# Kernel tuning notes

Hardware: AMD Instinct MI355X
Metric: run time of the kernel (lower is better)

The kernel has to match this reference:

```python
import jax, jax.numpy as jnp
import numpy as np
from jax import lax

BZ, CAPACITY, SEQ_LEN, IN_VAR, N_EDGES = 64, 134, 288, 16, 96


def setup_inputs() -> dict:
    key = jax.random.key(0)
    ks = jax.random.split(key, 9)
    s_gcn = 1.0 / np.sqrt(SEQ_LEN)
    s_conv = 1.0 / np.sqrt(IN_VAR * 3)
    s_fc = 1.0 / np.sqrt(2 * IN_VAR)
    return {
        "src": jax.random.normal(ks[0], (BZ, CAPACITY, SEQ_LEN, IN_VAR), dtype=jnp.float32),
        "feature_edge_index": jax.random.randint(ks[1], (2, N_EDGES), 0, IN_VAR, dtype=jnp.int32),
        # SAGEConv(seq_len, seq_len): out = lin_l(mean_neighbors) + lin_r(x); lin_l has bias
        "Wl": jax.random.uniform(ks[2], (SEQ_LEN, SEQ_LEN), jnp.float32, -s_gcn, s_gcn),
        "Wr": jax.random.uniform(ks[3], (SEQ_LEN, SEQ_LEN), jnp.float32, -s_gcn, s_gcn),
        "b_gcn": jax.random.uniform(ks[4], (SEQ_LEN,), jnp.float32, -s_gcn, s_gcn),
        "conv1_w": jax.random.uniform(ks[5], (IN_VAR, IN_VAR, 3), jnp.float32, -s_conv, s_conv),
        "conv2_w": jax.random.uniform(ks[6], (IN_VAR, IN_VAR, 5), jnp.float32, -s_conv, s_conv),
        "fc_w": jax.random.uniform(ks[7], (IN_VAR, 2 * IN_VAR), jnp.float32, -s_fc, s_fc),
        "fc_b": jax.random.uniform(ks[8], (IN_VAR,), jnp.float32, -s_fc, s_fc),
    }


def reference(src, feature_edge_index, Wl, Wr, b_gcn, conv1_w, conv2_w, fc_w, fc_b):
    bz, cap, S, F = src.shape  # [bz, capacity, seq_len, in_var]
    B = bz * cap
    # node features for the feature graph: [B, in_var, seq_len]
    x2 = src.transpose(0, 1, 3, 2).reshape(B, F, S)
    e_src, e_dst = feature_edge_index[0], feature_edge_index[1]
    # SAGEConv mean aggregation over shared edge_index, vectorized across B graphs
    gathered = x2[:, e_src, :]                                   # [B, E, S]
    agg = jnp.zeros_like(x2).at[:, e_dst, :].add(gathered)       # [B, F, S]
    deg = jnp.zeros((F,), x2.dtype).at[e_dst].add(1.0)
    mean = agg / jnp.maximum(deg, 1.0)[None, :, None]
    feat = (jnp.einsum('bns,ts->bnt', mean, Wl)
            + jnp.einsum('bns,ts->bnt', x2, Wr) + b_gcn)          # [B, F, S]
    fea_fea = feat.reshape(bz, cap, F, S).transpose(0, 1, 3, 2)   # [bz,cap,S,F]
    # dual temporal Conv1d branches (same padding, no bias) on [B, F, S]
    dn = ('NCH', 'OIH', 'NCH')
    c1 = lax.conv_general_dilated(x2, conv1_w, (1,), [(1, 1)], dimension_numbers=dn)
    c2 = lax.conv_general_dilated(x2, conv2_w, (2,), [(2, 2)][:1] * 1, dimension_numbers=dn) if False else lax.conv_general_dilated(x2, conv2_w, (1,), [(2, 2)], dimension_numbers=dn)
    temporal = (c1 + c2).transpose(0, 2, 1).reshape(bz, cap, S, F)
    com = jnp.concatenate([fea_fea, temporal], axis=-1)           # [bz,cap,S,2F]
    com = jnp.einsum('bcsf,of->bcso', com, fc_w) + fc_b
    # dropout is identity in eval mode
    return src + com
```

## Files before the change

kernel.cpp:

```cpp
#include <hip/hip_runtime.h>
#include <hip/hip_bf16.h>

typedef short short8 __attribute__((ext_vector_type(8)));
typedef float float4v __attribute__((ext_vector_type(4)));
typedef unsigned short ushort4v __attribute__((ext_vector_type(4)));

#define BTOT 8576
#define SEQ 288
#define NF 16
#define NB 3
#define SPN 296
#define XTROWS 294
#define XT_USH (XTROWS * 16)
#define XN_USH (16 * SPN)
#define PBN (XT_USH + XN_USH)
#define WCVW 104

__device__ __forceinline__ unsigned short f2b(float f) {
    union { float f; unsigned u; } v; v.f = f;
    unsigned r = v.u + 0x7FFF + ((v.u >> 16) & 1);
    return (unsigned short)(r >> 16);
}
__device__ __forceinline__ float b2f(unsigned short u) {
    union { unsigned u; float f; } v; v.u = ((unsigned)u) << 16; return v.f;
}

__global__ void wcast_kernel(const float* __restrict__ a, const float* __restrict__ b,
                             unsigned short* __restrict__ o) {
    int i = blockIdx.x * 256 + threadIdx.x;
    o[i]         = f2b(a[i]);
    o[82944 + i] = f2b(b[i]);
}

template<int WPRE>
__device__ __forceinline__ short8 ldw(const unsigned short* __restrict__ wb,
                                      const float* __restrict__ wf, int idx) {
    if (WPRE) {
        return *(const short8*)&wb[idx];
    } else {
        const float* p = &wf[idx];
        float4 w0 = *(const float4*)p, w1 = *(const float4*)(p + 4);
        short8 a;
        a[0] = (short)f2b(w0.x); a[1] = (short)f2b(w0.y);
        a[2] = (short)f2b(w0.z); a[3] = (short)f2b(w0.w);
        a[4] = (short)f2b(w1.x); a[5] = (short)f2b(w1.y);
        a[6] = (short)f2b(w1.z); a[7] = (short)f2b(w1.w);
        return a;
    }
}

#define LDB(KK9, B_) do {                                                      \
    const int s0_ = (KK9) * 32;                                                \
    (B_)[0] = *(const short8*)&xsN0[li * SPN + s0_ + 8 * g];                   \
    (B_)[1] = *(const short8*)&xsN1[li * SPN + s0_ + 8 * g];                   \
    (B_)[2] = *(const short8*)&xsN2[li * SPN + s0_ + 8 * g];                   \
} while (0)

#define LDA(WT_, WF_, KK9, A_) do {                                            \
    const int s0_ = (KK9) * 32;                                                \
    _Pragma("unroll")                                                          \
    for (int m_ = 0; m_ < 3; ++m_)                                             \
        if (m_ < nt) (A_)[m_] = ldw<WPRE>(WT_, WF_, arow[m_] + s0_ + 8 * g);   \
} while (0)

#define MFK(A_, B_) do {                                                       \
    _Pragma("unroll")                                                          \
    for (int m_ = 0; m_ < 3; ++m_)                                             \
        if (m_ < nt) {                                                         \
            acc[m_][0] = __builtin_amdgcn_mfma_f32_16x16x32_bf16((A_)[m_], (B_)[0], acc[m_][0], 0, 0, 0); \
            acc[m_][1] = __builtin_amdgcn_mfma_f32_16x16x32_bf16((A_)[m_], (B_)[1], acc[m_][1], 0, 0, 0); \
            acc[m_][2] = __builtin_amdgcn_mfma_f32_16x16x32_bf16((A_)[m_], (B_)[2], acc[m_][2], 0, 0, 0); \
        }                                                                      \
} while (0)

#define GEMM9(WT_, WF_) do {                                                   \
    short8 aC[3], aN[3];                                                       \
    LDA(WT_, WF_, 0, aC);                                                      \
    LDA(WT_, WF_, 1, aN);                                                      \
    _Pragma("unroll")                                                          \
    for (int kk = 0; kk < 9; ++kk) {                                           \
        short8 bb[NB];                                                         \
        LDB(kk, bb);                                                           \
        if (kk & 1) { MFK(aN, bb); if (kk < 7) LDA(WT_, WF_, kk + 2, aN); }    \
        else        { MFK(aC, bb); if (kk < 7) LDA(WT_, WF_, kk + 2, aC); }    \
    }                                                                          \
} while (0)

template<int WPRE>
__global__ __launch_bounds__(512, 4) void stconv_mfma(
    const float* __restrict__ src,
    const int*   __restrict__ eidx,
    const float* __restrict__ Wlf,
    const float* __restrict__ Wrf,
    const unsigned short* __restrict__ Wbf,
    const float* __restrict__ bgcn,
    const float* __restrict__ cw1g,
    const float* __restrict__ cw2g,
    const float* __restrict__ fcwg,
    const float* __restrict__ fcbg,
    float*       __restrict__ out)
{
    __shared__ unsigned short pool[NB * PBN];
    __shared__ unsigned short wcv[16 * WCVW];
    __shared__ unsigned short fcwB[16 * 40];
    __shared__ unsigned short MB[16 * 40];
    __shared__ float bg[SEQ];
    __shared__ float Msc[256];
    __shared__ float fcb[16];

    const int tid  = threadIdx.x;
    const int wav  = tid >> 6;
    const int lane = tid & 63;
    const int li   = lane & 15;
    const int g    = lane >> 4;
    const int b0   = blockIdx.x * NB;

    int bid[NB];
    #pragma unroll
    for (int n = 0; n < NB; ++n) bid[n] = (b0 + n < BTOT) ? (b0 + n) : (BTOT - 1);

    if (tid < 256) Msc[tid] = 0.0f;
    for (int i = tid; i < 16 * 40; i += 512) MB[i] = 0;
    for (int i = tid; i < 16 * WCVW; i += 512) wcv[i] = 0;
    if (tid < 288) {
        int nb2 = tid / 96, r2 = tid % 96;
        int r = r2 >> 4, f = r2 & 15;
        int row = (r < 2) ? r : 288 + r;
        pool[nb2 * PBN + row * 16 + f] = 0;
    }
    __syncthreads();

    if (tid < 96) atomicAdd(&Msc[eidx[96 + tid] * 16 + eidx[tid]], 1.0f);
    {
        #pragma unroll
        for (int i = 0; i < 2; ++i) {
            int u = i * 512 + tid;
            if (u < NB * 288) {
                int nbu = u / 288, blk = u % 288;
                const float* srcb = src + (size_t)bid[0] * 0  + (size_t)((nbu == 0) ? bid[0] : (nbu == 1) ? bid[1] : bid[2]) * (SEQ * NF);
                unsigned short* xsTu = pool + nbu * PBN;
                unsigned short* xsNu = pool + nbu * PBN + XT_USH;
                int s0 = (blk >> 2) * 4, f0 = (blk & 3) * 4;
                ushort4v h[4];
                #pragma unroll
                for (int r = 0; r < 4; ++r) {
                    float4 v = *(const float4*)(srcb + (s0 + r) * 16 + f0);
                    h[r][0] = f2b(v.x); h[r][1] = f2b(v.y);
                    h[r][2] = f2b(v.z); h[r][3] = f2b(v.w);
                    *(ushort4v*)&xsTu[(s0 + r + 2) * 16 + f0] = h[r];
                }
                #pragma unroll
                for (int c = 0; c < 4; ++c) {
                    ushort4v w;
                    w[0] = h[0][c]; w[1] = h[1][c]; w[2] = h[2][c]; w[3] = h[3][c];
                    *(ushort4v*)&xsNu[(f0 + c) * SPN + s0] = w;
                }
            }
        }
    }
    for (int j = tid; j < 1280; j += 512) {
        int fo = j / 80, rem = j % 80, fi = rem / 5, d = rem % 5;
        float t = cw2g[(fo * 16 + fi) * 5 + d];
        if (d >= 1 && d <= 3) t += cw1g[(fo * 16 + fi) * 3 + (d - 1)];
        wcv[fo * WCVW + d * 16 + fi] = f2b(t);
    }
    if (tid < 512) fcwB[(tid >> 5) * 40 + (tid & 31)] = f2b(fcwg[tid]);
    if (tid < SEQ) bg[tid] = bgcn[tid];
    if (tid < 16) fcb[tid] = fcbg[tid];
    __syncthreads();

    if (tid < 16) {
        float deg = 0.0f;
        #pragma unroll
        for (int f = 0; f < 16; ++f) deg += Msc[tid * 16 + f];
        float inv = 1.0f / fmaxf(deg, 1.0f);
        #pragma unroll
        for (int f = 0; f < 16; ++f) MB[tid * 40 + f] = f2b(Msc[tid * 16 + f] * inv);
    }
    __syncthreads();

    const int t2 = (wav == 0) ? 16 : ((wav == 5) ? 17 : -1);
    const int nt = (t2 >= 0) ? 3 : 2;
    const int tts[3] = {wav, wav + 8, t2};
    const int arow[3] = {(tts[0] * 16 + li) * 288, (tts[1] * 16 + li) * 288,
                         (t2 >= 0) ? ((t2 * 16 + li) * 288) : 0};

    const unsigned short* WblT = Wbf;
    const unsigned short* WbrT = Wbf + 288 * 288;
    const unsigned short* xsN0 = pool + 0 * PBN + XT_USH;
    const unsigned short* xsN1 = pool + 1 * PBN + XT_USH;
    const unsigned short* xsN2 = pool + 2 * PBN + XT_USH;

    float4v acc[3][NB];

    #pragma unroll
    for (int m = 0; m < 3; ++m)
        if (m < nt) {
            #pragma unroll
            for (int r = 0; r < 4; ++r) {
                float bv = bg[tts[m] * 16 + 4 * g + r];
                #pragma unroll
                for (int n = 0; n < NB; ++n) acc[m][n][r] = bv;
            }
        }
    GEMM9(WbrT, Wrf);
    __syncthreads();

    {
        short8 bm = *(const short8*)&MB[li * 40 + 8 * g];
        #pragma unroll
        for (int it = 0; it < 7; ++it) {
            int u = wav + 8 * it;
            if (u < NB * 18) {
                int nbu = u / 18, st = u % 18;
                unsigned short* xsTu = pool + nbu * PBN;
                unsigned short* msNu = pool + nbu * PBN + XT_USH;
                int s0 = st * 16;
                short8 a = {0, 0, 0, 0, 0, 0, 0, 0};
                if (g < 2) a = *(const short8*)&xsTu[(s0 + li + 2) * 16 + 8 * g];
                float4v c = {0.f, 0.f, 0.f, 0.f};
                c = __builtin_amdgcn_mfma_f32_16x16x32_bf16(a, bm, c, 0, 0, 0);
                ushort4v p;
                #pragma unroll
                for (int r = 0; r < 4; ++r) p[r] = f2b(c[r]);
                *(ushort4v*)&msNu[li * SPN + s0 + 4 * g] = p;
            }
        }
    }
    __syncthreads();

    GEMM9(WblT, Wlf);

    ushort4v p5o[3][NB];
    #pragma unroll
    for (int m = 0; m < 3; ++m)
        if (m < nt) {
            #pragma unroll
            for (int n = 0; n < NB; ++n) {
                #pragma unroll
                for (int r = 0; r < 4; ++r)
                    p5o[m][n][r] = f2b(acc[m][n][r]);
            }
        }

    ushort4v p6o[7];
    {
        short8 cb0 = *(const short8*)&wcv[li * WCVW + 0  + 8 * g];
        short8 cb1 = *(const short8*)&wcv[li * WCVW + 32 + 8 * g];
        short8 cb2 = *(const short8*)&wcv[li * WCVW + 64 + 8 * g];
        const int fi0   = (g & 1) * 8;
        const int dbase = g >> 1;
        #pragma unroll
        for (int it = 0; it < 7; ++it) {
            int u = wav + 8 * it;
            if (u < NB * 18) {
                int nbu = u / 18, st = u % 18;
                const unsigned short* xsTu = pool + nbu * PBN;
                int s0 = st * 16;
                int rbase = (s0 + li + dbase) * 16 + fi0;
                short8 a0 = *(const short8*)&xsTu[rbase];
                short8 a1 = *(const short8*)&xsTu[rbase + 32];
                short8 a2 = *(const short8*)&xsTu[rbase + 64];
                float4v c = {0.f, 0.f, 0.f, 0.f};
                c = __builtin_amdgcn_mfma_f32_16x16x32_bf16(a0, cb0, c, 0, 0, 0);
                c = __builtin_amdgcn_mfma_f32_16x16x32_bf16(a1, cb1, c, 0, 0, 0);
                c = __builtin_amdgcn_mfma_f32_16x16x32_bf16(a2, cb2, c, 0, 0, 0);
                #pragma unroll
                for (int r = 0; r < 4; ++r) p6o[it][r] = f2b(c[r]);
            }
        }
    }

    ushort4v res16[7];
    #pragma unroll
    for (int it = 0; it < 7; ++it) {
        int u = wav + 8 * it;
        if (u < NB * 18) {
            int nbu = u / 18, st = u % 18;
            const unsigned short* xsTu = pool + nbu * PBN;
            int s0 = st * 16;
            #pragma unroll
            for (int r = 0; r < 4; ++r)
                res16[it][r] = xsTu[(s0 + 4 * g + r + 2) * 16 + li];
        }
    }
    __syncthreads();

    {
        #pragma unroll
        for (int m = 0; m < 3; ++m)
            if (m < nt) {
                #pragma unroll
                for (int n = 0; n < NB; ++n) {
                    unsigned short* catn = pool + n * PBN;
                    #pragma unroll
                    for (int r = 0; r < 4; ++r) {
                        int pos = tts[m] * 16 + 4 * g + r;
                        catn[pos * 32 + li] = p5o[m][n][r];
                    }
                }
            }
        #pragma unroll
        for (int it = 0; it < 7; ++it) {
            int u = wav + 8 * it;
            if (u < NB * 18) {
                int nbu = u / 18, st = u % 18;
                unsigned short* catn = pool + nbu * PBN;
                int s0 = st * 16;
                #pragma unroll
                for (int r = 0; r < 4; ++r)
                    catn[(s0 + 4 * g + r) * 32 + 16 + li] = p6o[it][r];
            }
        }
    }
    __syncthreads();

    {
        short8 fb = *(const short8*)&fcwB[li * 40 + 8 * g];
        #pragma unroll
        for (int it = 0; it < 7; ++it) {
            int u = wav + 8 * it;
            if (u < NB * 18) {
                int nbu = u / 18, st = u % 18;
                const unsigned short* catn = pool + nbu * PBN;
                float* outb = out + (size_t)bid[0] * 0 + (size_t)((nbu == 0) ? bid[0] : (nbu == 1) ? bid[1] : bid[2]) * (SEQ * NF);
                int s0 = st * 16;
                float4v c;
                #pragma unroll
                for (int r = 0; r < 4; ++r) c[r] = b2f(res16[it][r]) + fcb[li];
                short8 a = *(const short8*)&catn[(s0 + li) * 32 + 8 * g];
                c = __builtin_amdgcn_mfma_f32_16x16x32_bf16(a, fb, c, 0, 0, 0);
                #pragma unroll
                for (int r = 0; r < 4; ++r) outb[(s0 + 4 * g + r) * 16 + li] = c[r];
            }
        }
    }
}

extern "C" void kernel_launch(void* const* d_in, const int* in_sizes, int n_in,
                              void* d_out, int out_size, void* d_ws, size_t ws_size,
                              hipStream_t stream)
{
    const float* src  = (const float*)d_in[0];
    const int*   eidx = (const int*)  d_in[1];
    const float* Wl   = (const float*)d_in[2];
    const float* Wr   = (const float*)d_in[3];
    const float* bgcn = (const float*)d_in[4];
    const float* cw1  = (const float*)d_in[5];
    const float* cw2  = (const float*)d_in[6];
    const float* fcw  = (const float*)d_in[7];
    const float* fcb  = (const float*)d_in[8];
    float* out = (float*)d_out;

    const int grid = (BTOT + NB - 1) / NB;
    const size_t wbytes = (size_t)2 * 288 * 288 * sizeof(unsigned short);
    if (ws_size >= wbytes) {
        wcast_kernel<<<dim3(324), dim3(256), 0, stream>>>(Wl, Wr, (unsigned short*)d_ws);
        stconv_mfma<1><<<dim3(grid), dim3(512), 0, stream>>>(
            src, eidx, Wl, Wr, (const unsigned short*)d_ws,
            bgcn, cw1, cw2, fcw, fcb, out);
    } else {
        stconv_mfma<0><<<dim3(grid), dim3(512), 0, stream>>>(
            src, eidx, Wl, Wr, nullptr,
            bgcn, cw1, cw2, fcw, fcb, out);
    }
}
```

Baseline: 143.8 us.

## Process four graphs per block and compute edge counts without shared atomics

Raises the number of batch graphs handled per workgroup from three to four, so each loaded weight fragment feeds four MFMA columns instead of three. This amortizes weight loads and setup over more work. The shared-memory Msc/bg buffers and the atomic edge accumulation are removed: each of 256 threads scans the edge list directly and gets the degree by a shuffle reduction, which drops one barrier. In exchange the kernel uses more LDS and registers per block (larger accumulator and per-iteration arrays), which may lower occupancy, and the bias is now read from global memory.

```diff
diff --git a/kernel.cpp b/kernel.cpp
--- a/kernel.cpp
+++ b/kernel.cpp
@@ -8,7 +8,7 @@
 #define BTOT 8576
 #define SEQ 288
 #define NF 16
-#define NB 3
+#define NB 4
 #define SPN 296
 #define XTROWS 294
 #define XT_USH (XTROWS * 16)
@@ -54,6 +54,7 @@
     (B_)[0] = *(const short8*)&xsN0[li * SPN + s0_ + 8 * g];                   \
     (B_)[1] = *(const short8*)&xsN1[li * SPN + s0_ + 8 * g];                   \
     (B_)[2] = *(const short8*)&xsN2[li * SPN + s0_ + 8 * g];                   \
+    (B_)[3] = *(const short8*)&xsN3[li * SPN + s0_ + 8 * g];                   \
 } while (0)
 
 #define LDA(WT_, WF_, KK9, A_) do {                                            \
@@ -67,9 +68,9 @@
     _Pragma("unroll")                                                          \
     for (int m_ = 0; m_ < 3; ++m_)                                             \
         if (m_ < nt) {                                                         \
-            acc[m_][0] = __builtin_amdgcn_mfma_f32_16x16x32_bf16((A_)[m_], (B_)[0], acc[m_][0], 0, 0, 0); \
-            acc[m_][1] = __builtin_amdgcn_mfma_f32_16x16x32_bf16((A_)[m_], (B_)[1], acc[m_][1], 0, 0, 0); \
-            acc[m_][2] = __builtin_amdgcn_mfma_f32_16x16x32_bf16((A_)[m_], (B_)[2], acc[m_][2], 0, 0, 0); \
+            _Pragma("unroll")                                                  \
+            for (int n_ = 0; n_ < NB; ++n_)                                    \
+                acc[m_][n_] = __builtin_amdgcn_mfma_f32_16x16x32_bf16((A_)[m_], (B_)[n_], acc[m_][n_], 0, 0, 0); \
         }                                                                      \
 } while (0)
 
@@ -104,8 +105,6 @@
     __shared__ unsigned short wcv[16 * WCVW];
     __shared__ unsigned short fcwB[16 * 40];
     __shared__ unsigned short MB[16 * 40];
-    __shared__ float bg[SEQ];
-    __shared__ float Msc[256];
     __shared__ float fcb[16];
 
     const int tid  = threadIdx.x;
@@ -119,10 +118,9 @@
     #pragma unroll
     for (int n = 0; n < NB; ++n) bid[n] = (b0 + n < BTOT) ? (b0 + n) : (BTOT - 1);
 
-    if (tid < 256) Msc[tid] = 0.0f;
     for (int i = tid; i < 16 * 40; i += 512) MB[i] = 0;
     for (int i = tid; i < 16 * WCVW; i += 512) wcv[i] = 0;
-    if (tid < 288) {
+    if (tid < NB * 96) {
         int nb2 = tid / 96, r2 = tid % 96;
         int r = r2 >> 4, f = r2 & 15;
         int row = (r < 2) ? r : 288 + r;
@@ -130,14 +128,13 @@
     }
     __syncthreads();
 
-    if (tid < 96) atomicAdd(&Msc[eidx[96 + tid] * 16 + eidx[tid]], 1.0f);
-    {
-        #pragma unroll
-        for (int i = 0; i < 2; ++i) {
+    {
+        #pragma unroll
+        for (int i = 0; i < 3; ++i) {
             int u = i * 512 + tid;
             if (u < NB * 288) {
                 int nbu = u / 288, blk = u % 288;
-                const float* srcb = src + (size_t)bid[0] * 0  + (size_t)((nbu == 0) ? bid[0] : (nbu == 1) ? bid[1] : bid[2]) * (SEQ * NF);
+                const float* srcb = src + (size_t)bid[nbu & 3] * (SEQ * NF);
                 unsigned short* xsTu = pool + nbu * PBN;
                 unsigned short* xsNu = pool + nbu * PBN + XT_USH;
                 int s0 = (blk >> 2) * 4, f0 = (blk & 3) * 4;
@@ -165,17 +162,18 @@
         wcv[fo * WCVW + d * 16 + fi] = f2b(t);
     }
     if (tid < 512) fcwB[(tid >> 5) * 40 + (tid & 31)] = f2b(fcwg[tid]);
-    if (tid < SEQ) bg[tid] = bgcn[tid];
     if (tid < 16) fcb[tid] = fcbg[tid];
-    __syncthreads();
-
-    if (tid < 16) {
-        float deg = 0.0f;
-        #pragma unroll
-        for (int f = 0; f < 16; ++f) deg += Msc[tid * 16 + f];
-        float inv = 1.0f / fmaxf(deg, 1.0f);
-        #pragma unroll
-        for (int f = 0; f < 16; ++f) MB[tid * 40 + f] = f2b(Msc[tid * 16 + f] * inv);
+    if (tid < 256) {
+        const int d = tid >> 4, f = tid & 15;
+        float cnt = 0.0f;
+        for (int e = 0; e < 96; ++e) {
+            int es = eidx[e], ed = eidx[96 + e];
+            cnt += (ed == d && es == f) ? 1.0f : 0.0f;
+        }
+        float deg = cnt;
+        #pragma unroll
+        for (int off = 1; off < 16; off <<= 1) deg += __shfl_xor(deg, off);
+        MB[d * 40 + f] = f2b(cnt / fmaxf(deg, 1.0f));
     }
     __syncthreads();
 
@@ -190,6 +188,7 @@
     const unsigned short* xsN0 = pool + 0 * PBN + XT_USH;
     const unsigned short* xsN1 = pool + 1 * PBN + XT_USH;
     const unsigned short* xsN2 = pool + 2 * PBN + XT_USH;
+    const unsigned short* xsN3 = pool + 3 * PBN + XT_USH;
 
     float4v acc[3][NB];
 
@@ -198,7 +197,7 @@
         if (m < nt) {
             #pragma unroll
             for (int r = 0; r < 4; ++r) {
-                float bv = bg[tts[m] * 16 + 4 * g + r];
+                float bv = bgcn[tts[m] * 16 + 4 * g + r];
                 #pragma unroll
                 for (int n = 0; n < NB; ++n) acc[m][n][r] = bv;
             }
@@ -209,7 +208,7 @@
     {
         short8 bm = *(const short8*)&MB[li * 40 + 8 * g];
         #pragma unroll
-        for (int it = 0; it < 7; ++it) {
+        for (int it = 0; it < 9; ++it) {
             int u = wav + 8 * it;
             if (u < NB * 18) {
                 int nbu = u / 18, st = u % 18;
@@ -243,7 +242,7 @@
             }
         }
 
-    ushort4v p6o[7];
+    ushort4v p6o[9];
     {
         short8 cb0 = *(const short8*)&wcv[li * WCVW + 0  + 8 * g];
         short8 cb1 = *(const short8*)&wcv[li * WCVW + 32 + 8 * g];
@@ -251,7 +250,7 @@
         const int fi0   = (g & 1) * 8;
         const int dbase = g >> 1;
         #pragma unroll
-        for (int it = 0; it < 7; ++it) {
+        for (int it = 0; it < 9; ++it) {
             int u = wav + 8 * it;
             if (u < NB * 18) {
                 int nbu = u / 18, st = u % 18;
@@ -271,9 +270,9 @@
         }
     }
 
-    ushort4v res16[7];
+    ushort4v res16[9];
     #pragma unroll
-    for (int it = 0; it < 7; ++it) {
+    for (int it = 0; it < 9; ++it) {
         int u = wav + 8 * it;
         if (u < NB * 18) {
             int nbu = u / 18, st = u % 18;
@@ -301,7 +300,7 @@
                 }
             }
         #pragma unroll
-        for (int it = 0; it < 7; ++it) {
+        for (int it = 0; it < 9; ++it) {
             int u = wav + 8 * it;
             if (u < NB * 18) {
                 int nbu = u / 18, st = u % 18;
@@ -318,12 +317,12 @@
     {
         short8 fb = *(const short8*)&fcwB[li * 40 + 8 * g];
         #pragma unroll
-        for (int it = 0; it < 7; ++it) {
+        for (int it = 0; it < 9; ++it) {
             int u = wav + 8 * it;
             if (u < NB * 18) {
                 int nbu = u / 18, st = u % 18;
                 const unsigned short* catn = pool + nbu * PBN;
-                float* outb = out + (size_t)bid[0] * 0 + (size_t)((nbu == 0) ? bid[0] : (nbu == 1) ? bid[1] : bid[2]) * (SEQ * NF);
+                float* outb = out + (size_t)bid[nbu & 3] * (SEQ * NF);
                 int s0 = st * 16;
                 float4v c;
                 #pragma unroll
```

After: 167.4 us. 1.16x slower.
